# Kernel optimization log

Hardware: AMD Instinct MI355X
Metric: run time of the kernel (lower is better)

## Reference

```python
import jax, jax.numpy as jnp
import numpy as np
from math import factorial, sqrt

# ---------- real Wigner-3j coefficients (e3nn conventions) ----------

def _su2_cg(j1, j2, j3, m1, m2, m3):
    # Racah formula for integer angular momenta (complex Clebsch-Gordan).
    if m3 != m1 + m2:
        return 0.0
    f = factorial
    pre = sqrt((2 * j3 + 1) * f(j3 + j1 - j2) * f(j3 - j1 + j2) * f(j1 + j2 - j3)
               * f(j3 + m3) * f(j3 - m3)
               / (f(j1 + j2 + j3 + 1) * f(j1 - m1) * f(j1 + m1) * f(j2 - m2) * f(j2 + m2)))
    S = 0.0
    for v in range(0, j1 + j2 + j3 + 1):
        a = [v, j3 - j1 + j2 - v, j3 + m3 - v, v + j1 - j2 - m3, j2 + j3 + m1 - v, j1 - m1 + v]
        if any(t < 0 for t in a):
            continue
        S += (-1) ** (v + j2 + m2) * f(j2 + j3 + m1 - v) * f(j1 - m1 + v) \
             / (f(v) * f(j3 - j1 + j2 - v) * f(j3 + m3 - v) * f(v + j1 - j2 - m3))
    return pre * S


def _q_real_to_complex(l):
    # e3nn change_basis_real_to_complex
    q = np.zeros((2 * l + 1, 2 * l + 1), dtype=np.complex128)
    for m in range(-l, 0):
        q[l + m, l + abs(m)] = 1 / np.sqrt(2)
        q[l + m, l - abs(m)] = -1j / np.sqrt(2)
    q[l, l] = 1.0
    for m in range(1, l + 1):
        q[l + m, l + abs(m)] = (-1) ** m / np.sqrt(2)
        q[l + m, l - abs(m)] = 1j * (-1) ** m / np.sqrt(2)
    return (-1j) ** l * q  # phase that makes the real-basis 3j real


def _w3j(l1, l2, l3):
    C = np.zeros((2 * l1 + 1, 2 * l2 + 1, 2 * l3 + 1), dtype=np.complex128)
    for m1 in range(-l1, l1 + 1):
        for m2 in range(-l2, l2 + 1):
            m3 = m1 + m2
            if abs(m3) <= l3:
                C[l1 + m1, l2 + m2, l3 + m3] = _su2_cg(l1, l2, l3, m1, m2, m3)
    Q1, Q2, Q3 = _q_real_to_complex(l1), _q_real_to_complex(l2), _q_real_to_complex(l3)
    C = np.einsum('ij,kl,mn,ikn->jlm', Q1, Q2, np.conj(Q3.T), C)
    C = np.real(C)
    return (C / np.linalg.norm(C)).astype(np.float32)  # unit-norm real 3j

# ---------- FullyConnectedTensorProduct paths for irreps 0e+1o+2e (x) 0e+1o+2e -> 0e+1o+2e ----------
L = 2
DIM = (L + 1) ** 2  # 9
LS = list(range(L + 1))
PATHS = [(a, b, c) for a in LS for b in LS for c in LS
         if abs(a - b) <= c <= a + b and (a + b + c) % 2 == 0]
_FANIN = {c: sum(1 for p in PATHS if p[2] == c) for c in LS}
# path blocks already include component/element normalization sqrt(dim_out / fan_in)
BLOCKS = [_w3j(a, b, c) * np.sqrt((2 * c + 1) / _FANIN[c]) for (a, b, c) in PATHS]

E, CH = 262144, 64


def setup_inputs() -> dict:
    key = jax.random.key(0)
    kx, ky, kw, k1, k2, k3, k4 = jax.random.split(key, 7)
    bound = 1.0 / np.sqrt(DIM)  # nn.Linear default init bound
    return {
        "x": jax.random.normal(kx, (E, CH, DIM), dtype=jnp.float32),
        "y": jax.random.normal(ky, (E, CH, DIM), dtype=jnp.float32),
        "tp_w": jax.random.normal(kw, (len(PATHS),), dtype=jnp.float32),
        "Wfx": jax.random.uniform(k1, (DIM, DIM), jnp.float32, -bound, bound),
        "bfx": jax.random.uniform(k2, (DIM,), jnp.float32, -bound, bound),
        "Wfy": jax.random.uniform(k3, (DIM, DIM), jnp.float32, -bound, bound),
        "bfy": jax.random.uniform(k4, (DIM,), jnp.float32, -bound, bound),
    }


def reference(x, y, tp_w, Wfx, bfx, Wfy, bfy):
    # Assemble the weighted CG contraction tensor [9,9,9] from the 11 paths.
    C = jnp.zeros((DIM, DIM, DIM), dtype=x.dtype)
    for idx, (a, b, c) in enumerate(PATHS):
        blk = jnp.asarray(BLOCKS[idx])
        C = C.at[a * a:a * a + 2 * a + 1,
                 b * b:b * b + 2 * b + 1,
                 c * c:c * c + 2 * c + 1].add(tp_w[idx] * blk)
    # fused fully-connected tensor product over all edges/channels
    out = jnp.einsum('eci,ecj,ijk->eck', x, y, C)
    # fc branches: Linear(9,9) applied to flattened (edge*channel, 9)
    out = out + x @ Wfx.T + bfx + y @ Wfy.T + bfy
    return out  # [E, CH, 9]
```

## Files before the change

kernel.cpp:

```cpp
#include <hip/hip_runtime.h>

namespace cg {

constexpr double csqrt(double x) {
    double g = x < 1.0 ? 1.0 : x;
    for (int i = 0; i < 64; ++i) g = 0.5 * (g + x / g);
    return g;
}
constexpr double fact(int n) { double r = 1.0; for (int i = 2; i <= n; ++i) r *= (double)i; return r; }

constexpr double su2cg(int j1, int j2, int j3, int m1, int m2, int m3) {
    if (m1 + m2 != m3) return 0.0;
    double pre = csqrt((2.0*j3+1.0)*fact(j3+j1-j2)*fact(j3-j1+j2)*fact(j1+j2-j3)
                       *fact(j3+m3)*fact(j3-m3)
                       /(fact(j1+j2+j3+1)*fact(j1-m1)*fact(j1+m1)*fact(j2-m2)*fact(j2+m2)));
    double S = 0.0;
    for (int v = 0; v <= j1 + j2 + j3; ++v) {
        int b1 = j3-j1+j2-v, b2 = j3+m3-v, b3 = v+j1-j2-m3, b4 = j2+j3+m1-v, b5 = j1-m1+v;
        if (b1 < 0 || b2 < 0 || b3 < 0 || b4 < 0 || b5 < 0) continue;
        double term = fact(b4)*fact(b5)/(fact(v)*fact(b1)*fact(b2)*fact(b3));
        S += ((v + j2 + m2) & 1) ? -term : term;
    }
    return pre * S;
}

struct CD { double re, im; };
constexpr CD cmul(CD a, CD b) { return { a.re*b.re - a.im*b.im, a.re*b.im + a.im*b.re }; }

constexpr CD qent(int l, int r, int c) {
    const double s = 0.70710678118654752440;
    CD v{0.0, 0.0};
    int m = r - l;
    if (m < 0)       { if (c == l - m) v = { s, 0.0 }; else if (c == l + m) v = { 0.0, -s }; }
    else if (m == 0) { if (c == l)     v = { 1.0, 0.0 }; }
    else             { double sg = (m & 1) ? -1.0 : 1.0;
                       if (c == l + m) v = { sg*s, 0.0 }; else if (c == l - m) v = { 0.0, sg*s }; }
    if      (l == 1) v = { v.im, -v.re };
    else if (l == 2) v = { -v.re, -v.im };
    return v;
}

constexpr int PA_[11] = {0,0,0,1,1,1,1,2,2,2,2};
constexpr int PB_[11] = {0,1,2,0,1,1,2,0,1,2,2};
constexpr int PC_[11] = {0,1,2,1,0,2,1,2,1,0,2};
constexpr double FAN_[3] = {3.0, 4.0, 4.0};

struct KTab { float v[9][9][9]; };

constexpr KTab buildK() {
    KTab T{};
    for (int p = 0; p < 11; ++p) {
        const int a = PA_[p], b = PB_[p], c = PC_[p];
        double cgt[5][5] = {};
        for (int i = 0; i < 2*a+1; ++i)
            for (int k = 0; k < 2*b+1; ++k) {
                int m3 = (i-a) + (k-b);
                cgt[i][k] = (m3 >= -c && m3 <= c) ? su2cg(a,b,c,i-a,k-b,m3) : 0.0;
            }
        double R[5][5][5] = {};
        double nrm = 0.0;
        for (int j = 0; j < 2*a+1; ++j)
            for (int l = 0; l < 2*b+1; ++l)
                for (int m = 0; m < 2*c+1; ++m) {
                    double re = 0.0;
                    for (int i = 0; i < 2*a+1; ++i)
                        for (int k = 0; k < 2*b+1; ++k) {
                            double g = cgt[i][k];
                            if (g == 0.0) continue;
                            int n = (i-a) + (k-b) + c;
                            CD t12 = cmul(qent(a,i,j), qent(b,k,l));
                            CD q3  = qent(c,n,m);
                            re += (t12.re*q3.re + t12.im*q3.im) * g;
                        }
                    R[j][l][m] = re;
                    nrm += re*re;
                }
        double sc = csqrt((2.0*c+1.0)/FAN_[c]) / csqrt(nrm);
        for (int j = 0; j < 2*a+1; ++j)
            for (int l = 0; l < 2*b+1; ++l)
                for (int m = 0; m < 2*c+1; ++m)
                    T.v[a*a+j][b*b+l][c*c+m] = (float)(R[j][l][m] * sc);
    }
    return T;
}

constexpr KTab KT = buildK();

constexpr bool pairNZ(int p, int di, int dj) {
    const int a = PA_[p], b = PB_[p], c = PC_[p];
    for (int dk = 0; dk < 2 * c + 1; ++dk)
        if (KT.v[a*a+di][b*b+dj][c*c+dk] != 0.0f) return true;
    return false;
}

}


#define BLK 256
#define TPV 2

typedef float f4 __attribute__((ext_vector_type(4)));
typedef float f2 __attribute__((ext_vector_type(2)));

__global__ __launch_bounds__(BLK)
__attribute__((amdgpu_num_vgpr(128)))
void tp_main_kernel(
        const float* __restrict__ x, const float* __restrict__ y,
        float* __restrict__ out, const float* __restrict__ tpw,
        const float* __restrict__ Wfx, const float* __restrict__ bfx,
        const float* __restrict__ Wfy, const float* __restrict__ bfy)
{
    __shared__ __align__(16) float Wx[9][12];
    __shared__ __align__(16) float Wy[9][12];
    __shared__ float bs[9];

    const int t = threadIdx.x;

    if (t < 81) { Wx[t / 9][t % 9] = Wfx[t]; Wy[t / 9][t % 9] = Wfy[t]; }
    if (t < 9)  bs[t] = bfx[t] + bfy[t];

    float w[11];
    #pragma unroll
    for (int p = 0; p < 11; ++p) {
        union { float f; int i; } u;
        u.f = tpw[p];
        u.i = __builtin_amdgcn_readfirstlane(u.i);
        w[p] = u.f;
    }

    __syncthreads();

    const long set = (long)blockIdx.x * BLK + t;

    const float* xb = x + set * 18;
    const float* yb = y + set * 18;

    float xs[18], ys[18];
    #pragma unroll
    for (int q = 0; q < 4; ++q) {
        f4 a = *reinterpret_cast<const f4*>(xb + q * 4);
        xs[q*4+0] = a[0]; xs[q*4+1] = a[1]; xs[q*4+2] = a[2]; xs[q*4+3] = a[3];
        f4 b = *reinterpret_cast<const f4*>(yb + q * 4);
        ys[q*4+0] = b[0]; ys[q*4+1] = b[1]; ys[q*4+2] = b[2]; ys[q*4+3] = b[3];
    }
    {
        f2 a = *reinterpret_cast<const f2*>(xb + 16);
        xs[16] = a[0]; xs[17] = a[1];
        f2 b = *reinterpret_cast<const f2*>(yb + 16);
        ys[16] = b[0]; ys[17] = b[1];
    }

    float acc[18];
    #pragma unroll
    for (int k = 0; k < 9; ++k) {
        float bb = bs[k];
        acc[k] = bb; acc[9 + k] = bb;
    }

    #pragma unroll
    for (int k = 0; k < 9; ++k) {
        f4 wxa = *reinterpret_cast<const f4*>(&Wx[k][0]);
        f4 wxb = *reinterpret_cast<const f4*>(&Wx[k][4]);
        float wx8 = Wx[k][8];
        f4 wya = *reinterpret_cast<const f4*>(&Wy[k][0]);
        f4 wyb = *reinterpret_cast<const f4*>(&Wy[k][4]);
        float wy8 = Wy[k][8];
        #pragma unroll
        for (int v = 0; v < TPV; ++v) {
            float s = acc[v * 9 + k];
            #pragma unroll
            for (int i = 0; i < 4; ++i) {
                s += wxa[i] * xs[v * 9 + i]     + wya[i] * ys[v * 9 + i];
                s += wxb[i] * xs[v * 9 + 4 + i] + wyb[i] * ys[v * 9 + 4 + i];
            }
            s += wx8 * xs[v * 9 + 8] + wy8 * ys[v * 9 + 8];
            acc[v * 9 + k] = s;
        }
    }

    #pragma unroll
    for (int p = 0; p < 11; ++p) {
        const int a = cg::PA_[p], b = cg::PB_[p], c = cg::PC_[p];
        #pragma unroll
        for (int di = 0; di < 2 * a + 1; ++di) {
            #pragma unroll
            for (int dj = 0; dj < 2 * b + 1; ++dj) {
                if (cg::pairNZ(p, di, dj)) {
                    const int i = a * a + di, j = b * b + dj;
                    float prw[TPV];
                    #pragma unroll
                    for (int v = 0; v < TPV; ++v)
                        prw[v] = (xs[v * 9 + i] * ys[v * 9 + j]) * w[p];
                    #pragma unroll
                    for (int dk = 0; dk < 2 * c + 1; ++dk) {
                        const float kv = cg::KT.v[i][j][c * c + dk];
                        if (kv != 0.0f) {
                            #pragma unroll
                            for (int v = 0; v < TPV; ++v)
                                acc[v * 9 + c * c + dk] += kv * prw[v];
                        }
                    }
                }
            }
        }
    }

    float* ob = out + set * 18;
    #pragma unroll
    for (int q = 0; q < 4; ++q) {
        f4 o;
        o[0] = acc[q*4+0]; o[1] = acc[q*4+1]; o[2] = acc[q*4+2]; o[3] = acc[q*4+3];
        *reinterpret_cast<f4*>(ob + q * 4) = o;
    }
    {
        f2 o;
        o[0] = acc[16]; o[1] = acc[17];
        *reinterpret_cast<f2*>(ob + 16) = o;
    }
}


extern "C" void kernel_launch(void* const* d_in, const int* in_sizes, int n_in,
                              void* d_out, int out_size, void* d_ws, size_t ws_size,
                              hipStream_t stream) {
    const float* x   = (const float*)d_in[0];
    const float* y   = (const float*)d_in[1];
    const float* tpw = (const float*)d_in[2];
    const float* Wfx = (const float*)d_in[3];
    const float* bfx = (const float*)d_in[4];
    const float* Wfy = (const float*)d_in[5];
    const float* bfy = (const float*)d_in[6];
    float* out = (float*)d_out;

    long n_items = (long)out_size / 9;
    long n_sets = n_items / TPV;
    long grid = n_sets / BLK;

    hipLaunchKernelGGL(tp_main_kernel, dim3((unsigned)grid), dim3(BLK), 0, stream,
                       x, y, out, tpw, Wfx, bfx, Wfy, bfy);
}
```

Before: 421.5 us.

## Stage per-wavefront x/y loads and output stores through LDS for coalescing

Each wavefront now loads its contiguous 64×18-float tile of x and y into shared memory with fully contiguous float4 global loads. Each lane then reads its own 18 floats back from LDS. The results are written to the same LDS region and copied out to global memory with contiguous float4 stores. The goal is to replace the 72-byte-strided per-thread global accesses with fully coalesced transactions, at the cost of about 36KB of LDS per block (which may lower occupancy) and possible LDS bank conflicts on the strided reads.

```diff
diff --git a/kernel.cpp b/kernel.cpp
--- a/kernel.cpp
+++ b/kernel.cpp
@@ -98,6 +98,7 @@
 
 #define BLK 256
 #define TPV 2
+#define WSL 1152
 
 typedef float f4 __attribute__((ext_vector_type(4)));
 typedef float f2 __attribute__((ext_vector_type(2)));
@@ -110,43 +111,66 @@
         const float* __restrict__ Wfx, const float* __restrict__ bfx,
         const float* __restrict__ Wfy, const float* __restrict__ bfy)
 {
+    __shared__ __align__(16) float L[4][2 * WSL];
     __shared__ __align__(16) float Wx[9][12];
     __shared__ __align__(16) float Wy[9][12];
     __shared__ float bs[9];
 
     const int t = threadIdx.x;
+    const int w = t >> 6;
+    const int lane = t & 63;
 
     if (t < 81) { Wx[t / 9][t % 9] = Wfx[t]; Wy[t / 9][t % 9] = Wfy[t]; }
     if (t < 9)  bs[t] = bfx[t] + bfy[t];
 
-    float w[11];
+    float pw[11];
     #pragma unroll
     for (int p = 0; p < 11; ++p) {
         union { float f; int i; } u;
         u.f = tpw[p];
         u.i = __builtin_amdgcn_readfirstlane(u.i);
-        w[p] = u.f;
+        pw[p] = u.f;
     }
 
     __syncthreads();
 
-    const long set = (long)blockIdx.x * BLK + t;
-
-    const float* xb = x + set * 18;
-    const float* yb = y + set * 18;
+    const long gw = (long)blockIdx.x * 4 + w;
+    const f4* xg4 = reinterpret_cast<const f4*>(x)   + gw * 288;
+    const f4* yg4 = reinterpret_cast<const f4*>(y)   + gw * 288;
+    f4*       og4 = reinterpret_cast<f4*>(out)       + gw * 288;
+
+    float* Lw = L[w];
+    f4* Lx4 = reinterpret_cast<f4*>(Lw);
+    f4* Ly4 = reinterpret_cast<f4*>(Lw + WSL);
+
+    {
+        f4 tx0 = xg4[lane];        f4 tx1 = xg4[lane + 64];
+        f4 tx2 = xg4[lane + 128];  f4 tx3 = xg4[lane + 192];
+        f4 ty0 = yg4[lane];        f4 ty1 = yg4[lane + 64];
+        f4 ty2 = yg4[lane + 128];  f4 ty3 = yg4[lane + 192];
+        f4 tx4, ty4;
+        if (lane < 32) { tx4 = xg4[lane + 256]; ty4 = yg4[lane + 256]; }
+        Lx4[lane] = tx0;       Lx4[lane + 64] = tx1;
+        Lx4[lane + 128] = tx2; Lx4[lane + 192] = tx3;
+        Ly4[lane] = ty0;       Ly4[lane + 64] = ty1;
+        Ly4[lane + 128] = ty2; Ly4[lane + 192] = ty3;
+        if (lane < 32) { Lx4[lane + 256] = tx4; Ly4[lane + 256] = ty4; }
+    }
 
     float xs[18], ys[18];
-    #pragma unroll
-    for (int q = 0; q < 4; ++q) {
-        f4 a = *reinterpret_cast<const f4*>(xb + q * 4);
-        xs[q*4+0] = a[0]; xs[q*4+1] = a[1]; xs[q*4+2] = a[2]; xs[q*4+3] = a[3];
-        f4 b = *reinterpret_cast<const f4*>(yb + q * 4);
-        ys[q*4+0] = b[0]; ys[q*4+1] = b[1]; ys[q*4+2] = b[2]; ys[q*4+3] = b[3];
-    }
-    {
-        f2 a = *reinterpret_cast<const f2*>(xb + 16);
+    {
+        const float* px = Lw + lane * 18;
+        const float* py = Lw + WSL + lane * 18;
+        #pragma unroll
+        for (int q = 0; q < 4; ++q) {
+            f4 a = *reinterpret_cast<const f4*>(px + q * 4);
+            xs[q*4+0] = a[0]; xs[q*4+1] = a[1]; xs[q*4+2] = a[2]; xs[q*4+3] = a[3];
+            f4 b = *reinterpret_cast<const f4*>(py + q * 4);
+            ys[q*4+0] = b[0]; ys[q*4+1] = b[1]; ys[q*4+2] = b[2]; ys[q*4+3] = b[3];
+        }
+        f2 a = *reinterpret_cast<const f2*>(px + 16);
         xs[16] = a[0]; xs[17] = a[1];
-        f2 b = *reinterpret_cast<const f2*>(yb + 16);
+        f2 b = *reinterpret_cast<const f2*>(py + 16);
         ys[16] = b[0]; ys[17] = b[1];
     }
 
@@ -190,7 +214,7 @@
                     float prw[TPV];
                     #pragma unroll
                     for (int v = 0; v < TPV; ++v)
-                        prw[v] = (xs[v * 9 + i] * ys[v * 9 + j]) * w[p];
+                        prw[v] = (xs[v * 9 + i] * ys[v * 9 + j]) * pw[p];
                     #pragma unroll
                     for (int dk = 0; dk < 2 * c + 1; ++dk) {
                         const float kv = cg::KT.v[i][j][c * c + dk];
@@ -205,17 +229,25 @@
         }
     }
 
-    float* ob = out + set * 18;
-    #pragma unroll
-    for (int q = 0; q < 4; ++q) {
-        f4 o;
-        o[0] = acc[q*4+0]; o[1] = acc[q*4+1]; o[2] = acc[q*4+2]; o[3] = acc[q*4+3];
-        *reinterpret_cast<f4*>(ob + q * 4) = o;
-    }
-    {
+    {
+        float* px = Lw + lane * 18;
+        #pragma unroll
+        for (int q = 0; q < 4; ++q) {
+            f4 o;
+            o[0] = acc[q*4+0]; o[1] = acc[q*4+1]; o[2] = acc[q*4+2]; o[3] = acc[q*4+3];
+            *reinterpret_cast<f4*>(px + q * 4) = o;
+        }
         f2 o;
         o[0] = acc[16]; o[1] = acc[17];
-        *reinterpret_cast<f2*>(ob + 16) = o;
+        *reinterpret_cast<f2*>(px + 16) = o;
+    }
+
+    {
+        og4[lane]       = Lx4[lane];
+        og4[lane + 64]  = Lx4[lane + 64];
+        og4[lane + 128] = Lx4[lane + 128];
+        og4[lane + 192] = Lx4[lane + 192];
+        if (lane < 32) og4[lane + 256] = Lx4[lane + 256];
     }
 }
 
```

Result: slower. 437.8 us (+3.9%).
